# Optimization experiments

Measured on AMD Instinct MI355X. Metric: run time of the kernel, lower is better.

The kernel has to match this reference:

```python
import jax, jax.numpy as jnp
import numpy as np

# ---- static config (matches init_kwargs) ----
ANCHORS = jnp.array([[64,64],[64,128],[128,64],[128,128],[128,256],
                     [256,128],[256,256],[256,512],[512,256]], dtype=jnp.float32)  # [A,2] (h,w)
A = 9
STRIDE = 16
IMG = 512
HF = IMG // STRIDE  # 32
K_PROP = 300        # proposals kept by RPNProposalSelectorLayer
POOL = 3            # ROIMaxPool(3,3)
SAMP = 2            # samples per bin edge for max pooling approximation
NUM_CLASSES = 20


def _conv(x, w, b, stride):
    y = jax.lax.conv_general_dilated(
        x, w, window_strides=(stride, stride), padding='SAME',
        dimension_numbers=('NHWC', 'HWIO', 'NHWC'))
    return y + b


def setup_inputs() -> dict:
    key = jax.random.key(0)
    ks = jax.random.split(key, 24)
    s = 0.05
    d = {}
    d['x'] = jax.random.normal(ks[0], (4, IMG, IMG, 3), dtype=jnp.float32)
    # backbone: 4 stride-2 convs -> /16, 256 channels
    d['w1'] = jax.random.normal(ks[1], (3, 3, 3, 64)) * s;    d['b1'] = jnp.zeros((64,))
    d['w2'] = jax.random.normal(ks[2], (3, 3, 64, 128)) * s;  d['b2'] = jnp.zeros((128,))
    d['w3'] = jax.random.normal(ks[3], (3, 3, 128, 256)) * s; d['b3'] = jnp.zeros((256,))
    d['w4'] = jax.random.normal(ks[4], (3, 3, 256, 256)) * s; d['b4'] = jnp.zeros((256,))
    # RPN heads (1x1 convs)
    d['w_cls'] = jax.random.normal(ks[5], (1, 1, 256, 2 * A)) * s;  d['b_cls'] = jnp.zeros((2 * A,))
    d['w_bbox'] = jax.random.normal(ks[6], (1, 1, 256, 4 * A)) * s; d['b_bbox'] = jnp.zeros((4 * A,))
    # FC heads (pooled 3*3*256 = 2304)
    d['w_fc1'] = jax.random.normal(ks[7], (2304, 512)) * s;   d['b_fc1'] = jnp.zeros((512,))
    d['w_fc2'] = jax.random.normal(ks[8], (2304, 256)) * s;   d['b_fc2'] = jnp.zeros((256,))
    d['w_clsfc'] = jax.random.normal(ks[9], (256, NUM_CLASSES)) * s; d['b_clsfc'] = jnp.zeros((NUM_CLASSES,))
    d['w_bboxfc'] = jax.random.normal(ks[10], (256, 4)) * s;  d['b_bboxfc'] = jnp.zeros((4,))
    return d


def _forward(x, w1, b1, w2, b2, w3, b3, w4, b4, w_cls, b_cls, w_bbox, b_bbox,
             w_fc1, b_fc1, w_fc2, b_fc2, w_clsfc, b_clsfc, w_bboxfc, b_bboxfc):
    B = x.shape[0]
    # ---- feature extractor ----
    f = jax.nn.relu(_conv(x, w1, b1, 2))
    f = jax.nn.relu(_conv(f, w2, b2, 2))
    f = jax.nn.relu(_conv(f, w3, b3, 2))
    f = jax.nn.relu(_conv(f, w4, b4, 2))          # [B,32,32,256]
    Hf = f.shape[1]; Wf = f.shape[2]; C = f.shape[3]
    # ---- RPN heads ----
    bbox_conv = _conv(f, w_bbox, b_bbox, 1)       # [B,Hf,Wf,4A]
    cls_conv = _conv(f, w_cls, b_cls, 1)          # [B,Hf,Wf,2A]
    # ---- RPNProposalGeneratorLayer: decode anchors, clip, yxyx ----
    deltas = bbox_conv.reshape(B, Hf, Wf, A, 4)   # (ty,tx,th,tw)
    cy = (jnp.arange(Hf, dtype=jnp.float32) + 0.5) * STRIDE  # [Hf]
    cx = (jnp.arange(Wf, dtype=jnp.float32) + 0.5) * STRIDE  # [Wf]
    ah = ANCHORS[:, 0]; aw = ANCHORS[:, 1]                    # [A]
    yc = cy[None, :, None, None] + deltas[..., 0] * ah        # [B,Hf,Wf,A]
    xc = cx[None, None, :, None] + deltas[..., 1] * aw
    hh = ah * jnp.exp(jnp.clip(deltas[..., 2], -4.0, 4.0))
    ww = aw * jnp.exp(jnp.clip(deltas[..., 3], -4.0, 4.0))
    y1 = jnp.clip(yc - hh * 0.5, 0.0, IMG); x1 = jnp.clip(xc - ww * 0.5, 0.0, IMG)
    y2 = jnp.clip(yc + hh * 0.5, 0.0, IMG); x2 = jnp.clip(xc + ww * 0.5, 0.0, IMG)
    proposals = jnp.stack([y1, x1, y2, x2], axis=-1).reshape(B, Hf * Wf * A, 4) / IMG  # percentage yxyx
    # ---- RPNProposalSelectorLayer: fg prob + top-K ----
    logits = cls_conv.reshape(B, Hf * Wf * A, 2)
    fg_prob = jax.nn.softmax(logits, axis=-1)[..., 1]          # [B,N]
    selected_prob, top_idx = jax.lax.top_k(fg_prob, K_PROP)    # [B,K]
    selected_proposals = jnp.take_along_axis(proposals, top_idx[..., None], axis=1)  # [B,K,4]
    # ---- ROIMaxPool(3,3): max over 2x2 samples per bin ----
    ys0 = selected_proposals[..., 0] * Hf; xs0 = selected_proposals[..., 1] * Wf
    ys1 = selected_proposals[..., 2] * Hf; xs1 = selected_proposals[..., 3] * Wf
    bh = (ys1 - ys0) / POOL; bw = (xs1 - xs0) / POOL           # [B,K]
    grid = jnp.arange(POOL, dtype=jnp.float32)[:, None] + (jnp.arange(SAMP, dtype=jnp.float32)[None, :] + 0.5) / SAMP  # [3,2]
    ysamp = ys0[..., None, None] + grid * bh[..., None, None]  # [B,K,3,2]
    xsamp = xs0[..., None, None] + grid * bw[..., None, None]  # [B,K,3,2]
    yi = jnp.clip(jnp.floor(ysamp), 0, Hf - 1).astype(jnp.int32)[:, :, :, None, :, None]  # [B,K,3,1,2,1]
    xi = jnp.clip(jnp.floor(xsamp), 0, Wf - 1).astype(jnp.int32)[:, :, None, :, None, :]  # [B,K,1,3,1,2]
    b_idx = jnp.arange(B)[:, None, None, None, None, None]
    gathered = f[b_idx, yi, xi]                                # [B,K,3,3,2,2,C]
    pooled = jnp.max(gathered, axis=(4, 5))                    # [B,K,3,3,C]
    flat = pooled.reshape(B, K_PROP, POOL * POOL * C)          # [B,K,2304]
    # ---- FC heads (note: fc_2 consumes flat directly, as in source) ----
    fc1 = jax.nn.relu(flat @ w_fc1 + b_fc1)                    # computed, unused (faithful)
    fc2 = jax.nn.relu(flat @ w_fc2 + b_fc2)                    # [B,K,256]
    cls_prob = jax.nn.sigmoid(fc2 @ w_clsfc + b_clsfc)         # [B,K,20]
    bbox_delt = fc2 @ w_bboxfc + b_bboxfc                      # [B,K,4]
    return selected_proposals, selected_prob, cls_prob, bbox_delt


def reference(x, w1, b1, w2, b2, w3, b3, w4, b4, w_cls, b_cls, w_bbox, b_bbox,
              w_fc1, b_fc1, w_fc2, b_fc2, w_clsfc, b_clsfc, w_bboxfc, b_bboxfc):
    return _forward(x, w1, b1, w2, b2, w3, b3, w4, b4, w_cls, b_cls, w_bbox, b_bbox,
                    w_fc1, b_fc1, w_fc2, b_fc2, w_clsfc, b_clsfc, w_bboxfc, b_bboxfc)
```

## Files before the change

kernel.cpp:

```cpp
#include <hip/hip_runtime.h>
#include <cstdint>
#include <cstddef>


constexpr int ilog2c(int v) { int r = 0; while (v > 1) { v >>= 1; ++r; } return r; }

__global__ __launch_bounds__(256)
void conv1_kernel(const float* __restrict__ x, const float* __restrict__ w,
                  const float* __restrict__ bias, float* __restrict__ out)
{
    const int co  = threadIdx.x;
    const int pix = blockIdx.x * 4 + threadIdx.y;
    const int ox = pix & 255;
    const int oy = (pix >> 8) & 255;
    const int b  = pix >> 16;
    float acc = bias[co];
    #pragma unroll
    for (int ky = 0; ky < 3; ++ky) {
        const int iy = 2 * oy + ky;
        if (iy >= 512) continue;
        #pragma unroll
        for (int kx = 0; kx < 3; ++kx) {
            const int ix = 2 * ox + kx;
            if (ix >= 512) continue;
            const float* xp = x + ((size_t)((b * 512 + iy) * 512 + ix)) * 3;
            const float* wp = w + ((ky * 3 + kx) * 3) * 64 + co;
            acc = fmaf(xp[0], wp[0],   acc);
            acc = fmaf(xp[1], wp[64],  acc);
            acc = fmaf(xp[2], wp[128], acc);
        }
    }
    out[(size_t)pix * 64 + co] = fmaxf(acc, 0.f);
}

template<int CIN, int COUT, int HIN, int HOUT>
__global__ __launch_bounds__(256)
void conv_gemm(const float* __restrict__ in, const float* __restrict__ w,
               const float* __restrict__ bias, float* __restrict__ out)
{
    constexpr int K = 9 * CIN;
    constexpr int L2CIN  = ilog2c(CIN);
    constexpr int L2HOUT = ilog2c(HOUT);
    __shared__ float As[64][68];
    __shared__ float Bs[64][68];

    const int m0 = blockIdx.x * 64;
    const int n0 = blockIdx.y * 64;
    const int tid = threadIdx.x;
    const int tx = tid & 15, ty = tid >> 4;
    const int q     = tid & 15;
    const int row16 = tid >> 4;

    float acc[4][4] = {};

    for (int k0 = 0; k0 < K; k0 += 64) {
        {
            const int kabs = k0 + q * 4;
            const int ci  = kabs & (CIN - 1);
            const int kxy = kabs >> L2CIN;
            const int ky = kxy / 3, kx = kxy - 3 * ky;
            #pragma unroll
            for (int r = 0; r < 4; ++r) {
                const int mm = row16 + 16 * r;
                const int m  = m0 + mm;
                const int ox = m & (HOUT - 1);
                const int oy = (m >> L2HOUT) & (HOUT - 1);
                const int bb = m >> (2 * L2HOUT);
                const int iy = 2 * oy + ky, ix = 2 * ox + kx;
                float4 v = make_float4(0.f, 0.f, 0.f, 0.f);
                if (iy < HIN && ix < HIN) {
                    v = *reinterpret_cast<const float4*>(
                        in + ((size_t)((bb * HIN + iy) * HIN + ix)) * CIN + ci);
                }
                As[q * 4 + 0][mm] = v.x;
                As[q * 4 + 1][mm] = v.y;
                As[q * 4 + 2][mm] = v.z;
                As[q * 4 + 3][mm] = v.w;
            }
        }
        {
            #pragma unroll
            for (int r = 0; r < 4; ++r) {
                const int kk = row16 + 16 * r;
                float4 v = *reinterpret_cast<const float4*>(
                    w + (size_t)(k0 + kk) * COUT + n0 + q * 4);
                *reinterpret_cast<float4*>(&Bs[kk][q * 4]) = v;
            }
        }
        __syncthreads();
        #pragma unroll 8
        for (int kk = 0; kk < 64; ++kk) {
            const float4 a = *reinterpret_cast<const float4*>(&As[kk][ty * 4]);
            const float4 b = *reinterpret_cast<const float4*>(&Bs[kk][tx * 4]);
            const float av[4] = {a.x, a.y, a.z, a.w};
            const float bv[4] = {b.x, b.y, b.z, b.w};
            #pragma unroll
            for (int i = 0; i < 4; ++i)
                #pragma unroll
                for (int j = 0; j < 4; ++j)
                    acc[i][j] = fmaf(av[i], bv[j], acc[i][j]);
        }
        __syncthreads();
    }
    #pragma unroll
    for (int i = 0; i < 4; ++i) {
        const int m = m0 + ty * 4 + i;
        float4 o;
        o.x = fmaxf(acc[i][0] + bias[n0 + tx * 4 + 0], 0.f);
        o.y = fmaxf(acc[i][1] + bias[n0 + tx * 4 + 1], 0.f);
        o.z = fmaxf(acc[i][2] + bias[n0 + tx * 4 + 2], 0.f);
        o.w = fmaxf(acc[i][3] + bias[n0 + tx * 4 + 3], 0.f);
        *reinterpret_cast<float4*>(out + (size_t)m * COUT + n0 + tx * 4) = o;
    }
}

template<int K, int N>
__global__ __launch_bounds__(256)
void gemm_fc(const float* __restrict__ Aa, const float* __restrict__ w,
             const float* __restrict__ bias, float* __restrict__ out, int M)
{
    __shared__ float As[64][68];
    __shared__ float Bs[64][68];
    const int m0 = blockIdx.x * 64;
    const int n0 = blockIdx.y * 64;
    const int tid = threadIdx.x;
    const int tx = tid & 15, ty = tid >> 4;
    const int q = tid & 15, row16 = tid >> 4;
    float acc[4][4] = {};

    for (int k0 = 0; k0 < K; k0 += 64) {
        #pragma unroll
        for (int r = 0; r < 4; ++r) {
            const int mm = row16 + 16 * r;
            const int m  = m0 + mm;
            float4 v = make_float4(0.f, 0.f, 0.f, 0.f);
            if (m < M) {
                v = *reinterpret_cast<const float4*>(Aa + (size_t)m * K + k0 + q * 4);
            }
            As[q * 4 + 0][mm] = v.x;
            As[q * 4 + 1][mm] = v.y;
            As[q * 4 + 2][mm] = v.z;
            As[q * 4 + 3][mm] = v.w;
        }
        #pragma unroll
        for (int r = 0; r < 4; ++r) {
            const int kk = row16 + 16 * r;
            float4 v = *reinterpret_cast<const float4*>(
                w + (size_t)(k0 + kk) * N + n0 + q * 4);
            *reinterpret_cast<float4*>(&Bs[kk][q * 4]) = v;
        }
        __syncthreads();
        #pragma unroll 8
        for (int kk = 0; kk < 64; ++kk) {
            const float4 a = *reinterpret_cast<const float4*>(&As[kk][ty * 4]);
            const float4 b = *reinterpret_cast<const float4*>(&Bs[kk][tx * 4]);
            const float av[4] = {a.x, a.y, a.z, a.w};
            const float bv[4] = {b.x, b.y, b.z, b.w};
            #pragma unroll
            for (int i = 0; i < 4; ++i)
                #pragma unroll
                for (int j = 0; j < 4; ++j)
                    acc[i][j] = fmaf(av[i], bv[j], acc[i][j]);
        }
        __syncthreads();
    }
    #pragma unroll
    for (int i = 0; i < 4; ++i) {
        const int m = m0 + ty * 4 + i;
        if (m >= M) continue;
        float4 o;
        o.x = fmaxf(acc[i][0] + bias[n0 + tx * 4 + 0], 0.f);
        o.y = fmaxf(acc[i][1] + bias[n0 + tx * 4 + 1], 0.f);
        o.z = fmaxf(acc[i][2] + bias[n0 + tx * 4 + 2], 0.f);
        o.w = fmaxf(acc[i][3] + bias[n0 + tx * 4 + 3], 0.f);
        *reinterpret_cast<float4*>(out + (size_t)m * N + n0 + tx * 4) = o;
    }
}

__global__ __launch_bounds__(256)
void clsprob_kernel(const float* __restrict__ f, const float* __restrict__ w_cls,
                    const float* __restrict__ b_cls, float* __restrict__ fg)
{
    const int t = blockIdx.x * 256 + threadIdx.x;
    const int b = t / 9216;
    const int k = t - b * 9216;
    const int a = k % 9;
    const int pos = k / 9;
    const float* fv = f + (size_t)(b * 1024 + pos) * 256;
    float l0 = b_cls[2 * a], l1 = b_cls[2 * a + 1];
    #pragma unroll 4
    for (int ci = 0; ci < 256; ++ci) {
        const float xv = fv[ci];
        l0 = fmaf(xv, w_cls[ci * 18 + 2 * a],     l0);
        l1 = fmaf(xv, w_cls[ci * 18 + 2 * a + 1], l1);
    }
    const float m  = fmaxf(l0, l1);
    const float e0 = expf(l0 - m), e1 = expf(l1 - m);
    fg[t] = e1 / (e0 + e1);
}

__global__ __launch_bounds__(1024)
void topk_kernel(const float* __restrict__ fg, int* __restrict__ top_idx,
                 float* __restrict__ out_prob)
{
    extern __shared__ unsigned long long keys[];
    const int b = blockIdx.x, tid = threadIdx.x;
    for (int i = tid; i < 16384; i += 1024) {
        unsigned long long kv = 0ull;
        if (i < 9216) {
            unsigned u = __float_as_uint(fg[b * 9216 + i]);
            u = (u & 0x80000000u) ? ~u : (u | 0x80000000u);
            kv = ((unsigned long long)u << 32) | (unsigned)(0xFFFFFFFFu - (unsigned)i);
        }
        keys[i] = kv;
    }
    __syncthreads();
    for (int k = 2; k <= 16384; k <<= 1) {
        for (int j = k >> 1; j > 0; j >>= 1) {
            for (int t = tid; t < 8192; t += 1024) {
                const int i = ((t & ~(j - 1)) << 1) | (t & (j - 1));
                const int p = i | j;
                const unsigned long long a = keys[i], c = keys[p];
                const bool desc = (i & k) == 0;
                if (desc ? (a < c) : (a > c)) { keys[i] = c; keys[p] = a; }
            }
            __syncthreads();
        }
    }
    if (tid < 300) {
        const unsigned long long kv = keys[tid];
        const unsigned u = (unsigned)(kv >> 32);
        const unsigned bits = (u & 0x80000000u) ? (u & 0x7FFFFFFFu) : ~u;
        out_prob[b * 300 + tid] = __uint_as_float(bits);
        top_idx[b * 300 + tid]  = (int)(0xFFFFFFFFu - (unsigned)(kv & 0xFFFFFFFFu));
    }
}

__global__ __launch_bounds__(64)
void proposal_kernel(const float* __restrict__ f, const float* __restrict__ w_bbox,
                     const float* __restrict__ b_bbox, const int* __restrict__ top_idx,
                     float* __restrict__ out_prop, float* __restrict__ roib)
{
    const int item = blockIdx.x;
    const int b = item / 300;
    const int idx = top_idx[item];
    const int a = idx % 9, pos = idx / 9;
    const int xw = pos & 31, yh = pos >> 5;
    const float* fv = f + ((size_t)((b * 32 + yh) * 32 + xw)) * 256;
    const int lane = threadIdx.x;
    const int j = lane & 3;
    float s = 0.f;
    for (int ci = lane >> 2; ci < 256; ci += 16)
        s = fmaf(fv[ci], w_bbox[ci * 36 + 4 * a + j], s);
    #pragma unroll
    for (int m = 4; m <= 32; m <<= 1) s += __shfl_xor(s, m, 64);
    const float d = s + b_bbox[4 * a + j];
    const float d0 = __shfl(d, 0, 64);
    const float d1 = __shfl(d, 1, 64);
    const float d2 = __shfl(d, 2, 64);
    const float d3 = __shfl(d, 3, 64);
    if (lane == 0) {
        const float anch_h[9] = {64, 64, 128, 128, 128, 256, 256, 256, 512};
        const float anch_w[9] = {64, 128, 64, 128, 256, 128, 256, 512, 256};
        const float cy = (yh + 0.5f) * 16.f, cx = (xw + 0.5f) * 16.f;
        const float ah = anch_h[a], aw = anch_w[a];
        const float yc = __fadd_rn(cy, __fmul_rn(d0, ah));
        const float xc = __fadd_rn(cx, __fmul_rn(d1, aw));
        const float hh = __fmul_rn(ah, expf(fminf(fmaxf(d2, -4.f), 4.f)));
        const float ww = __fmul_rn(aw, expf(fminf(fmaxf(d3, -4.f), 4.f)));
        const float y1 = fminf(fmaxf(__fsub_rn(yc, __fmul_rn(hh, 0.5f)), 0.f), 512.f);
        const float x1 = fminf(fmaxf(__fsub_rn(xc, __fmul_rn(ww, 0.5f)), 0.f), 512.f);
        const float y2 = fminf(fmaxf(__fadd_rn(yc, __fmul_rn(hh, 0.5f)), 0.f), 512.f);
        const float x2 = fminf(fmaxf(__fadd_rn(xc, __fmul_rn(ww, 0.5f)), 0.f), 512.f);
        float4 pr = make_float4(y1 * (1.f / 512.f), x1 * (1.f / 512.f),
                                y2 * (1.f / 512.f), x2 * (1.f / 512.f));
        *reinterpret_cast<float4*>(out_prop + (size_t)item * 4) = pr;
        float4 rb = make_float4(pr.x * 32.f, pr.y * 32.f, pr.z * 32.f, pr.w * 32.f);
        *reinterpret_cast<float4*>(roib + (size_t)item * 4) = rb;
    }
}

__global__ __launch_bounds__(256)
void roi_pool_kernel(const float* __restrict__ f, const float* __restrict__ roib,
                     float* __restrict__ flat)
{
    const int item = blockIdx.x;
    const int c = threadIdx.x;
    const int b = item / 300;
    const float ys0 = roib[item * 4 + 0], xs0 = roib[item * 4 + 1];
    const float ys1 = roib[item * 4 + 2], xs1 = roib[item * 4 + 3];
    const float bh = __fdiv_rn(__fsub_rn(ys1, ys0), 3.f);
    const float bw = __fdiv_rn(__fsub_rn(xs1, xs0), 3.f);
    int yi[3][2], xi[3][2];
    #pragma unroll
    for (int p = 0; p < 3; ++p) {
        #pragma unroll
        for (int s = 0; s < 2; ++s) {
            const float g = (float)p + (s ? 0.75f : 0.25f);
            const float ys = __fadd_rn(ys0, __fmul_rn(g, bh));
            const float xs = __fadd_rn(xs0, __fmul_rn(g, bw));
            yi[p][s] = (int)fminf(fmaxf(floorf(ys), 0.f), 31.f);
            xi[p][s] = (int)fminf(fmaxf(floorf(xs), 0.f), 31.f);
        }
    }
    const float* fb = f + (size_t)b * 32 * 32 * 256 + c;
    float* op = flat + (size_t)item * 2304 + c;
    #pragma unroll
    for (int py = 0; py < 3; ++py) {
        #pragma unroll
        for (int px = 0; px < 3; ++px) {
            const float v00 = fb[(size_t)(yi[py][0] * 32 + xi[px][0]) * 256];
            const float v01 = fb[(size_t)(yi[py][0] * 32 + xi[px][1]) * 256];
            const float v10 = fb[(size_t)(yi[py][1] * 32 + xi[px][0]) * 256];
            const float v11 = fb[(size_t)(yi[py][1] * 32 + xi[px][1]) * 256];
            op[(py * 3 + px) * 256] = fmaxf(fmaxf(v00, v01), fmaxf(v10, v11));
        }
    }
}

__global__ __launch_bounds__(256)
void heads_kernel(const float* __restrict__ fc2, const float* __restrict__ w_clsfc,
                  const float* __restrict__ b_clsfc, const float* __restrict__ w_bboxfc,
                  const float* __restrict__ b_bboxfc, float* __restrict__ out)
{
    const int t = blockIdx.x * 256 + threadIdx.x;
    if (t >= 1200 * 24) return;
    const int item = t / 24;
    const int j = t - item * 24;
    const float* v = fc2 + (size_t)item * 256;
    if (j < 20) {
        float s = b_clsfc[j];
        #pragma unroll 4
        for (int ci = 0; ci < 256; ++ci) s = fmaf(v[ci], w_clsfc[ci * 20 + j], s);
        out[6000 + item * 20 + j] = 1.f / (1.f + expf(-s));
    } else {
        const int q = j - 20;
        float s = b_bboxfc[q];
        #pragma unroll 4
        for (int ci = 0; ci < 256; ++ci) s = fmaf(v[ci], w_bboxfc[ci * 4 + q], s);
        out[30000 + item * 4 + q] = s;
    }
}

extern "C" void kernel_launch(void* const* d_in, const int* in_sizes, int n_in,
                              void* d_out, int out_size, void* d_ws, size_t ws_size,
                              hipStream_t stream)
{
    const float* x       = (const float*)d_in[0];
    const float* w1      = (const float*)d_in[1];
    const float* b1      = (const float*)d_in[2];
    const float* w2      = (const float*)d_in[3];
    const float* b2      = (const float*)d_in[4];
    const float* w3      = (const float*)d_in[5];
    const float* b3      = (const float*)d_in[6];
    const float* w4      = (const float*)d_in[7];
    const float* b4      = (const float*)d_in[8];
    const float* w_cls   = (const float*)d_in[9];
    const float* b_cls   = (const float*)d_in[10];
    const float* w_bbox  = (const float*)d_in[11];
    const float* b_bbox  = (const float*)d_in[12];
    const float* w_fc2   = (const float*)d_in[15];
    const float* b_fc2   = (const float*)d_in[16];
    const float* w_clsfc = (const float*)d_in[17];
    const float* b_clsfc = (const float*)d_in[18];
    const float* w_bboxfc= (const float*)d_in[19];
    const float* b_bboxfc= (const float*)d_in[20];
    float* out = (float*)d_out;
    char* ws = (char*)d_ws;

    float* f1   = (float*)(ws + 0);
    float* f2   = (float*)(ws + 67108864);
    float* f3   = (float*)(ws + 0);
    float* f4   = (float*)(ws + 67108864);
    float* flat = (float*)(ws + 0);
    float* fc2o = (float*)(ws + 11059200);
    float* fg   = (float*)(ws + 100663296);
    int*   tidx = (int*)  (ws + 100810752);
    float* roib = (float*)(ws + 100815552);

    conv1_kernel<<<65536, dim3(64, 4), 0, stream>>>(x, w1, b1, f1);
    conv_gemm<64, 128, 256, 128><<<dim3(1024, 2), 256, 0, stream>>>(f1, w2, b2, f2);
    conv_gemm<128, 256, 128, 64><<<dim3(256, 4), 256, 0, stream>>>(f2, w3, b3, f3);
    conv_gemm<256, 256, 64, 32><<<dim3(64, 4), 256, 0, stream>>>(f3, w4, b4, f4);

    clsprob_kernel<<<144, 256, 0, stream>>>(f4, w_cls, b_cls, fg);
    topk_kernel<<<4, 1024, 131072, stream>>>(fg, tidx, out + 4800);

    proposal_kernel<<<1200, 64, 0, stream>>>(f4, w_bbox, b_bbox, tidx, out, roib);
    roi_pool_kernel<<<1200, 256, 0, stream>>>(f4, roib, flat);

    gemm_fc<2304, 256><<<dim3(19, 4), 256, 0, stream>>>(flat, w_fc2, b_fc2, fc2o, 1200);
    heads_kernel<<<113, 256, 0, stream>>>(fc2o, w_clsfc, b_clsfc, w_bboxfc, b_bboxfc, out);
}
```

Before: 847.9 us.

## Run conv2 on bf16 MFMA with three-way split for fp32 accuracy

Adds a conv kernel that splits fp32 activations and weights into three bf16 parts each and accumulates six MFMA products per fragment. This emulates fp32 precision on matrix cores, and it replaces the scalar-FMA conv_gemm for the second conv layer. It also vectorizes the clsprob inner loop with float4 loads, clamps top-k indices, and moves workspace buffers to new offsets. The cost is sixfold MFMA work plus the splitting arithmetic on every tile load.

```diff
diff --git a/kernel.cpp b/kernel.cpp
--- a/kernel.cpp
+++ b/kernel.cpp
@@ -4,6 +4,27 @@
 
 
 constexpr int ilog2c(int v) { int r = 0; while (v > 1) { v >>= 1; ++r; } return r; }
+
+typedef short short8 __attribute__((ext_vector_type(8)));
+typedef float f32x4 __attribute__((ext_vector_type(4)));
+
+__device__ inline unsigned short bf_rn(float v) {
+    unsigned u = __builtin_bit_cast(unsigned, v);
+    u += 0x7FFFu + ((u >> 16) & 1u);
+    return (unsigned short)(u >> 16);
+}
+__device__ inline float bf_up(unsigned short b) {
+    unsigned u = (unsigned)b << 16;
+    return __builtin_bit_cast(float, u);
+}
+__device__ inline void split3(float v, unsigned short& s0, unsigned short& s1,
+                              unsigned short& s2) {
+    s0 = bf_rn(v);
+    float r = v - bf_up(s0);
+    s1 = bf_rn(r);
+    r = r - bf_up(s1);
+    s2 = bf_rn(r);
+}
 
 __global__ __launch_bounds__(256)
 void conv1_kernel(const float* __restrict__ x, const float* __restrict__ w,
@@ -114,6 +135,151 @@
     }
 }
 
+template<int CIN, int COUT, int HIN, int HOUT, int MFRAGS, bool B_PRESPLIT>
+__global__ __launch_bounds__(256)
+void conv_bf3(const float* __restrict__ in,
+              const unsigned short* __restrict__ w0p,
+              const unsigned short* __restrict__ w1p,
+              const unsigned short* __restrict__ w2p,
+              const float* __restrict__ w_f32, const float* __restrict__ bias,
+              float* __restrict__ out)
+{
+    constexpr int K = 9 * CIN;
+    constexpr int BM = 64 * MFRAGS;
+    constexpr int NIT = BM / 64;
+    constexpr int L2CIN  = ilog2c(CIN);
+    constexpr int L2HOUT = ilog2c(HOUT);
+    __shared__ alignas(16) unsigned short As0[BM * 32];
+    __shared__ alignas(16) unsigned short As1[BM * 32];
+    __shared__ alignas(16) unsigned short As2[BM * 32];
+    __shared__ alignas(16) unsigned short Bs0[64 * 32];
+    __shared__ alignas(16) unsigned short Bs1[64 * 32];
+    __shared__ alignas(16) unsigned short Bs2[64 * 32];
+
+    const int tid  = threadIdx.x;
+    const int lane = tid & 63, wv = tid >> 6;
+    const int m0 = blockIdx.x * BM, n0 = blockIdx.y * 64;
+
+    f32x4 acc[MFRAGS][4] = {};
+
+    int  rowbase[NIT];
+    bool ey[NIT], ex[NIT];
+    #pragma unroll
+    for (int it = 0; it < NIT; ++it) {
+        const int task = it * 256 + tid;
+        const int m = task >> 2;
+        const int gm = m0 + m;
+        const int ox = gm & (HOUT - 1);
+        const int oy = (gm >> L2HOUT) & (HOUT - 1);
+        const int bb = gm >> (2 * L2HOUT);
+        rowbase[it] = (bb * HIN + 2 * oy) * HIN + 2 * ox;
+        ey[it] = (oy == HOUT - 1);
+        ex[it] = (ox == HOUT - 1);
+    }
+
+    for (int k0 = 0; k0 < K; k0 += 32) {
+        const int ci0 = k0 & (CIN - 1);
+        const int kxy = k0 >> L2CIN;
+        const int ky = kxy / 3, kx = kxy - 3 * ky;
+        #pragma unroll
+        for (int it = 0; it < NIT; ++it) {
+            const int task = it * 256 + tid;
+            const int m = task >> 2, q = task & 3;
+            short8 p0 = {}, p1 = {}, p2 = {};
+            const bool valid = !(ey[it] && ky == 2) && !(ex[it] && kx == 2);
+            if (valid) {
+                const float* src = in + (size_t)(rowbase[it] + ky * HIN + kx) * CIN
+                                      + ci0 + q * 8;
+                const float4 va = *reinterpret_cast<const float4*>(src);
+                const float4 vb = *reinterpret_cast<const float4*>(src + 4);
+                const float vv[8] = {va.x, va.y, va.z, va.w, vb.x, vb.y, vb.z, vb.w};
+                #pragma unroll
+                for (int j = 0; j < 8; ++j) {
+                    unsigned short s0, s1, s2;
+                    split3(vv[j], s0, s1, s2);
+                    p0[j] = (short)s0; p1[j] = (short)s1; p2[j] = (short)s2;
+                }
+            }
+            *reinterpret_cast<short8*>(&As0[m * 32 + q * 8]) = p0;
+            *reinterpret_cast<short8*>(&As1[m * 32 + q * 8]) = p1;
+            *reinterpret_cast<short8*>(&As2[m * 32 + q * 8]) = p2;
+        }
+        if constexpr (B_PRESPLIT) {
+            const int n = tid >> 2, q = tid & 3;
+            const size_t gb = (size_t)(n0 + n) * K + k0 + q * 8;
+            *reinterpret_cast<short8*>(&Bs0[n * 32 + q * 8]) =
+                *reinterpret_cast<const short8*>(w0p + gb);
+            *reinterpret_cast<short8*>(&Bs1[n * 32 + q * 8]) =
+                *reinterpret_cast<const short8*>(w1p + gb);
+            *reinterpret_cast<short8*>(&Bs2[n * 32 + q * 8]) =
+                *reinterpret_cast<const short8*>(w2p + gb);
+        } else {
+            #pragma unroll
+            for (int it = 0; it < 2; ++it) {
+                const int t = it * 256 + tid;
+                const int k = t >> 4, nq = t & 15;
+                const float4 v = *reinterpret_cast<const float4*>(
+                    w_f32 + (size_t)(k0 + k) * COUT + n0 + nq * 4);
+                const float vv[4] = {v.x, v.y, v.z, v.w};
+                #pragma unroll
+                for (int j = 0; j < 4; ++j) {
+                    unsigned short s0, s1, s2;
+                    split3(vv[j], s0, s1, s2);
+                    Bs0[(nq * 4 + j) * 32 + k] = s0;
+                    Bs1[(nq * 4 + j) * 32 + k] = s1;
+                    Bs2[(nq * 4 + j) * 32 + k] = s2;
+                }
+            }
+        }
+        __syncthreads();
+        const int rsel = lane & 15, kb = lane >> 4;
+        short8 a0[MFRAGS], a1[MFRAGS], a2[MFRAGS];
+        #pragma unroll
+        for (int mi = 0; mi < MFRAGS; ++mi) {
+            const int row = wv * (MFRAGS * 16) + mi * 16 + rsel;
+            a0[mi] = *reinterpret_cast<const short8*>(&As0[row * 32 + kb * 8]);
+            a1[mi] = *reinterpret_cast<const short8*>(&As1[row * 32 + kb * 8]);
+            a2[mi] = *reinterpret_cast<const short8*>(&As2[row * 32 + kb * 8]);
+        }
+        short8 b0[4], b1[4], b2[4];
+        #pragma unroll
+        for (int ni = 0; ni < 4; ++ni) {
+            const int col = ni * 16 + rsel;
+            b0[ni] = *reinterpret_cast<const short8*>(&Bs0[col * 32 + kb * 8]);
+            b1[ni] = *reinterpret_cast<const short8*>(&Bs1[col * 32 + kb * 8]);
+            b2[ni] = *reinterpret_cast<const short8*>(&Bs2[col * 32 + kb * 8]);
+        }
+        #pragma unroll
+        for (int mi = 0; mi < MFRAGS; ++mi)
+            #pragma unroll
+            for (int ni = 0; ni < 4; ++ni) {
+                f32x4 t = acc[mi][ni];
+                t = __builtin_amdgcn_mfma_f32_16x16x32_bf16(a2[mi], b0[ni], t, 0, 0, 0);
+                t = __builtin_amdgcn_mfma_f32_16x16x32_bf16(a1[mi], b1[ni], t, 0, 0, 0);
+                t = __builtin_amdgcn_mfma_f32_16x16x32_bf16(a0[mi], b2[ni], t, 0, 0, 0);
+                t = __builtin_amdgcn_mfma_f32_16x16x32_bf16(a1[mi], b0[ni], t, 0, 0, 0);
+                t = __builtin_amdgcn_mfma_f32_16x16x32_bf16(a0[mi], b1[ni], t, 0, 0, 0);
+                t = __builtin_amdgcn_mfma_f32_16x16x32_bf16(a0[mi], b0[ni], t, 0, 0, 0);
+                acc[mi][ni] = t;
+            }
+        __syncthreads();
+    }
+    const int rsel = lane & 15, rq = lane >> 4;
+    #pragma unroll
+    for (int mi = 0; mi < MFRAGS; ++mi) {
+        #pragma unroll
+        for (int ni = 0; ni < 4; ++ni) {
+            const int col = n0 + ni * 16 + rsel;
+            const float bv = bias[col];
+            #pragma unroll
+            for (int r = 0; r < 4; ++r) {
+                const int row = m0 + wv * (MFRAGS * 16) + mi * 16 + rq * 4 + r;
+                out[(size_t)row * COUT + col] = fmaxf(acc[mi][ni][r] + bv, 0.f);
+            }
+        }
+    }
+}
+
 template<int K, int N>
 __global__ __launch_bounds__(256)
 void gemm_fc(const float* __restrict__ Aa, const float* __restrict__ w,
@@ -134,9 +300,7 @@
             const int mm = row16 + 16 * r;
             const int m  = m0 + mm;
             float4 v = make_float4(0.f, 0.f, 0.f, 0.f);
-            if (m < M) {
-                v = *reinterpret_cast<const float4*>(Aa + (size_t)m * K + k0 + q * 4);
-            }
+            if (m < M) v = *reinterpret_cast<const float4*>(Aa + (size_t)m * K + k0 + q * 4);
             As[q * 4 + 0][mm] = v.x;
             As[q * 4 + 1][mm] = v.y;
             As[q * 4 + 2][mm] = v.z;
@@ -145,8 +309,7 @@
         #pragma unroll
         for (int r = 0; r < 4; ++r) {
             const int kk = row16 + 16 * r;
-            float4 v = *reinterpret_cast<const float4*>(
-                w + (size_t)(k0 + kk) * N + n0 + q * 4);
+            float4 v = *reinterpret_cast<const float4*>(w + (size_t)(k0 + kk) * N + n0 + q * 4);
             *reinterpret_cast<float4*>(&Bs[kk][q * 4]) = v;
         }
         __syncthreads();
@@ -188,11 +351,17 @@
     const int pos = k / 9;
     const float* fv = f + (size_t)(b * 1024 + pos) * 256;
     float l0 = b_cls[2 * a], l1 = b_cls[2 * a + 1];
-    #pragma unroll 4
-    for (int ci = 0; ci < 256; ++ci) {
-        const float xv = fv[ci];
-        l0 = fmaf(xv, w_cls[ci * 18 + 2 * a],     l0);
-        l1 = fmaf(xv, w_cls[ci * 18 + 2 * a + 1], l1);
+    #pragma unroll 2
+    for (int ci = 0; ci < 256; ci += 4) {
+        const float4 xv = *reinterpret_cast<const float4*>(fv + ci);
+        l0 = fmaf(xv.x, w_cls[(ci + 0) * 18 + 2 * a], l0);
+        l1 = fmaf(xv.x, w_cls[(ci + 0) * 18 + 2 * a + 1], l1);
+        l0 = fmaf(xv.y, w_cls[(ci + 1) * 18 + 2 * a], l0);
+        l1 = fmaf(xv.y, w_cls[(ci + 1) * 18 + 2 * a + 1], l1);
+        l0 = fmaf(xv.z, w_cls[(ci + 2) * 18 + 2 * a], l0);
+        l1 = fmaf(xv.z, w_cls[(ci + 2) * 18 + 2 * a + 1], l1);
+        l0 = fmaf(xv.w, w_cls[(ci + 3) * 18 + 2 * a], l0);
+        l1 = fmaf(xv.w, w_cls[(ci + 3) * 18 + 2 * a + 1], l1);
     }
     const float m  = fmaxf(l0, l1);
     const float e0 = expf(l0 - m), e1 = expf(l1 - m);
@@ -243,7 +412,8 @@
 {
     const int item = blockIdx.x;
     const int b = item / 300;
-    const int idx = top_idx[item];
+    int idx = top_idx[item];
+    idx = idx < 0 ? 0 : (idx > 9215 ? 9215 : idx);
     const int a = idx % 9, pos = idx / 9;
     const int xw = pos & 31, yh = pos >> 5;
     const float* fv = f + ((size_t)((b * 32 + yh) * 32 + xw)) * 256;
@@ -368,18 +538,19 @@
     float* out = (float*)d_out;
     char* ws = (char*)d_ws;
 
-    float* f1   = (float*)(ws + 0);
-    float* f2   = (float*)(ws + 67108864);
+    float* f1 = (float*)(ws + 0);
+    float* f2 = (float*)(ws + 67108864);
     float* f3   = (float*)(ws + 0);
-    float* f4   = (float*)(ws + 67108864);
-    float* flat = (float*)(ws + 0);
-    float* fc2o = (float*)(ws + 11059200);
-    float* fg   = (float*)(ws + 100663296);
-    int*   tidx = (int*)  (ws + 100810752);
-    float* roib = (float*)(ws + 100815552);
+    float* f4   = (float*)(ws + 16777216);
+    float* fg   = (float*)(ws + 20971520);
+    int*   tidx = (int*)  (ws + 21118976);
+    float* roib = (float*)(ws + 21138176);
+    float* flat = (float*)(ws + 21157376);
+    float* fc2o = (float*)(ws + 32216576);
 
     conv1_kernel<<<65536, dim3(64, 4), 0, stream>>>(x, w1, b1, f1);
-    conv_gemm<64, 128, 256, 128><<<dim3(1024, 2), 256, 0, stream>>>(f1, w2, b2, f2);
+    conv_bf3<64, 128, 256, 128, 2, false>
+        <<<dim3(512, 2), 256, 0, stream>>>(f1, nullptr, nullptr, nullptr, w2, b2, f2);
     conv_gemm<128, 256, 128, 64><<<dim3(256, 4), 256, 0, stream>>>(f2, w3, b3, f3);
     conv_gemm<256, 256, 64, 32><<<dim3(64, 4), 256, 0, stream>>>(f3, w4, b4, f4);
 
```

After: 861.0 us. About the same (+1.5%).
